# Optimization experiments

Measured on AMD Instinct MI355X. Metric: run time of the kernel, lower is better.

Reference implementation:

```python
import jax, jax.numpy as jnp
import numpy as np

NCHARS = 50000
NWORDS = 500000
NIC = 64      # ninput_char
NIW = 64      # ninput_word
NH = 128      # nhidden
NA = 5        # naction (nmapping_fn)
B = 65536     # batch size


def setup_inputs() -> dict:
    key = jax.random.key(0)
    ks = jax.random.split(key, 12)
    s = 0.05
    return {
        "x": jax.random.randint(ks[0], (B, 2), 0, NCHARS),
        "y": jax.random.randint(ks[1], (B,), 0, NWORDS),
        "cemb_table": jax.random.normal(ks[2], (NCHARS, NIC), jnp.float32) * s,
        "wemb_table": jax.random.normal(ks[3], (NWORDS, NIW), jnp.float32) * s,
        # Policy MLP: Linear(2*NIC -> NH), ReLU, Linear(NH -> NA), Softmax
        "Wp1": jax.random.normal(ks[4], (2 * NIC, NH), jnp.float32) * s,
        "bp1": jnp.zeros((NH,), jnp.float32),
        "Wp2": jax.random.normal(ks[5], (NH, NA), jnp.float32) * s,
        "bp2": jnp.zeros((NA,), jnp.float32),
        # NA expert MLPs, stacked: Linear(2*NIC -> NH), ReLU, Linear(NH -> NIW)
        "We1": jax.random.normal(ks[6], (NA, 2 * NIC, NH), jnp.float32) * s,
        "be1": jnp.zeros((NA, NH), jnp.float32),
        "We2": jax.random.normal(ks[7], (NA, NH, NIW), jnp.float32) * s,
        "be2": jnp.zeros((NA, NIW), jnp.float32),
    }


def reference(x, y, cemb_table, wemb_table, Wp1, bp1, Wp2, bp2, We1, be1, We2, be2):
    bsize = x.shape[0]
    # char_embs(x).view(bsize, -1): [B, 2*NIC]
    cembs = cemb_table[x].reshape(bsize, -1)

    # Policy (dropout off in eval): probs = softmax(relu(cembs@Wp1+bp1)@Wp2+bp2)
    # Categorical sampling over probs == categorical over the pre-softmax logits.
    logits = jnp.maximum(cembs @ Wp1 + bp1, 0.0) @ Wp2 + bp2
    action = jax.random.categorical(jax.random.key(42), logits)   # [B]
    action_mask = jax.nn.one_hot(action, NA, dtype=cembs.dtype)   # [B, NA]

    # Dense evaluation of all NA experts (matches the Python loop + stack)
    h = jnp.maximum(jnp.einsum('bd,adh->bah', cembs, We1) + be1, 0.0)  # [B, NA, NH]
    mapped = jnp.einsum('bah,aho->bao', h, We2) + be2                  # [B, NA, NIW]

    # sum(unsqueeze(mask,-1) * mapped, dim=1)
    out = jnp.einsum('ba,bao->bo', action_mask, mapped)               # [B, NIW]

    wemb = wemb_table[y]                                              # [B, NIW]
    return (out, wemb)
```

## Files before the change

### kernel.cpp

```cpp
#include <hip/hip_runtime.h>
#include <stdint.h>

#define B_N   65536
#define NIC   64
#define NIW   64
#define NH    128
#define NA    5
#define D2    128

#define PARTITIONABLE 1

#define P2_NCHUNK 51
#define P2_R      1286

typedef __attribute__((ext_vector_type(8))) short short8;
typedef __attribute__((ext_vector_type(4))) float f32x4;

__device__ __forceinline__ ushort f2bf(float f) {
  uint32_t u = __float_as_uint(f);
  uint32_t r = (u + 0x7FFFu + ((u >> 16) & 1u)) >> 16;
  return (ushort)r;
}

__device__ __forceinline__ void split2(float f, ushort& h, ushort& l) {
  h = f2bf(f);
  l = f2bf(f - __uint_as_float(((uint32_t)h) << 16));
}

__device__ __forceinline__ void threefry2x32_k042(uint32_t x0, uint32_t x1,
                                                  uint32_t& o0, uint32_t& o1) {
  const uint32_t ks0 = 0u;
  const uint32_t ks1 = 42u;
  const uint32_t ks2 = 0x1BD11BDAu ^ 0u ^ 42u;
  x0 += ks0; x1 += ks1;
#define TF_RND(r) { x0 += x1; x1 = (x1 << (r)) | (x1 >> (32 - (r))); x1 ^= x0; }
  TF_RND(13) TF_RND(15) TF_RND(26) TF_RND(6)
  x0 += ks1; x1 += ks2 + 1u;
  TF_RND(17) TF_RND(29) TF_RND(16) TF_RND(24)
  x0 += ks2; x1 += ks0 + 2u;
  TF_RND(13) TF_RND(15) TF_RND(26) TF_RND(6)
  x0 += ks0; x1 += ks1 + 3u;
  TF_RND(17) TF_RND(29) TF_RND(16) TF_RND(24)
  x0 += ks1; x1 += ks2 + 4u;
  TF_RND(13) TF_RND(15) TF_RND(26) TF_RND(6)
  x0 += ks2; x1 += ks0 + 5u;
#undef TF_RND
  o0 = x0; o1 = x1;
}

__device__ __forceinline__ float gumbel_at(uint32_t idx) {
  uint32_t bits;
#if PARTITIONABLE
  uint32_t a, b;
  threefry2x32_k042(0u, idx, a, b);
  bits = a ^ b;
#else
  const uint32_t HALF = (uint32_t)(B_N * NA) / 2u;
  uint32_t a, b;
  if (idx < HALF) { threefry2x32_k042(idx, idx + HALF, a, b); bits = a; }
  else            { threefry2x32_k042(idx - HALF, idx, a, b); bits = b; }
#endif
  const float f = __uint_as_float((bits >> 9) | 0x3f800000u) - 1.0f;
  const double u = (f == 0.0f) ? (double)0x1p-126 : (double)f;
  const float nl = (float)(-log(u));
  const float g  = (float)(-log((double)nl));
  return g;
}

__global__ __launch_bounds__(512, 4) void policy_kernel(
    const int* __restrict__ x, const int* __restrict__ y,
    const float* __restrict__ cemb, const float* __restrict__ wemb,
    const float* __restrict__ Wp1, const float* __restrict__ bp1,
    const float* __restrict__ Wp2, const float* __restrict__ bp2,
    float* __restrict__ out_wemb, int* __restrict__ action) {
  __shared__ __align__(16) ushort sW1h[16384];
  __shared__ __align__(16) ushort sW1l[16384];
  __shared__ __align__(16) float sW2t[NA][NH];
  __shared__ __align__(16) float sb1[NH];
  __shared__ __align__(16) float sbp2[8];

  const int tid = threadIdx.x;
  const int base = blockIdx.x * 128;

  {
    const int n = tid & 127, q = tid >> 7;
    const int fb = (n >> 4) * 4 + q;
    const int cc = n & 15;
#pragma unroll
    for (int grp = 0; grp < 4; grp++) {
      short8 ph, pl;
#pragma unroll
      for (int j = 0; j < 8; j++) {
        const int k = 32 * q + 8 * grp + j;
        ushort hh, ll;
        split2(Wp1[k * NH + n], hh, ll);
        ph[j] = (short)hh;
        pl[j] = (short)ll;
      }
      *(short8*)&sW1h[fb * 512 + (cc + 16 * grp) * 8] = ph;
      *(short8*)&sW1l[fb * 512 + (cc + 16 * grp) * 8] = pl;
    }
    if (tid < NH) sb1[tid] = bp1[tid];
    if (tid < NA * 32) {
      const int a = tid >> 5, k0 = (tid & 31) * 4;
#pragma unroll
      for (int j = 0; j < 4; j++) sW2t[a][k0 + j] = Wp2[(k0 + j) * NA + a];
    }
    if (tid < NA) sbp2[tid] = bp2[tid];
  }

  const int wave = tid >> 6, lane = tid & 63;
  const int c16 = lane & 15, h2 = lane >> 4;

  const int grow = base + wave * 16 + c16;
  const int xi0 = x[grow * 2], xi1 = x[grow * 2 + 1];
  short8 Ah[4], Al[4];
#pragma unroll
  for (int kt = 0; kt < 4; kt++) {
    const int xi = (kt < 2) ? xi0 : xi1;
    const float* src = cemb + (size_t)xi * NIC + (kt & 1) * 32 + h2 * 8;
    const float4 aa = *(const float4*)src;
    const float4 bb = *(const float4*)(src + 4);
    ushort hh, ll;
    short8 ph, pl;
    split2(aa.x, hh, ll); ph[0] = (short)hh; pl[0] = (short)ll;
    split2(aa.y, hh, ll); ph[1] = (short)hh; pl[1] = (short)ll;
    split2(aa.z, hh, ll); ph[2] = (short)hh; pl[2] = (short)ll;
    split2(aa.w, hh, ll); ph[3] = (short)hh; pl[3] = (short)ll;
    split2(bb.x, hh, ll); ph[4] = (short)hh; pl[4] = (short)ll;
    split2(bb.y, hh, ll); ph[5] = (short)hh; pl[5] = (short)ll;
    split2(bb.z, hh, ll); ph[6] = (short)hh; pl[6] = (short)ll;
    split2(bb.w, hh, ll); ph[7] = (short)hh; pl[7] = (short)ll;
    Ah[kt] = ph;
    Al[kt] = pl;
  }
  __syncthreads();

  float part[4][5];
#pragma unroll
  for (int r = 0; r < 4; r++)
#pragma unroll
    for (int a = 0; a < NA; a++) part[r][a] = 0.0f;

#pragma unroll
  for (int half = 0; half < 2; half++) {
    f32x4 acc[4];
#pragma unroll
    for (int c2 = 0; c2 < 4; c2++) {
      const float bv = sb1[(half * 4 + c2) * 16 + c16];
      acc[c2] = (f32x4){bv, bv, bv, bv};
    }
#pragma unroll
    for (int kt = 0; kt < 4; kt++) {
#pragma unroll
      for (int c2 = 0; c2 < 4; c2++) {
        const int fb = (half * 4 + c2) * 4 + kt;
        const short8 Bh = *(const short8*)&sW1h[fb * 512 + lane * 8];
        const short8 Bl = *(const short8*)&sW1l[fb * 512 + lane * 8];
        acc[c2] = __builtin_amdgcn_mfma_f32_16x16x32_bf16(Ah[kt], Bh, acc[c2], 0, 0, 0);
        acc[c2] = __builtin_amdgcn_mfma_f32_16x16x32_bf16(Al[kt], Bh, acc[c2], 0, 0, 0);
        acc[c2] = __builtin_amdgcn_mfma_f32_16x16x32_bf16(Ah[kt], Bl, acc[c2], 0, 0, 0);
      }
    }
#pragma unroll
    for (int c2 = 0; c2 < 4; c2++) {
      const int ct = half * 4 + c2;
      float w[NA];
#pragma unroll
      for (int a = 0; a < NA; a++) w[a] = sW2t[a][ct * 16 + c16];
#pragma unroll
      for (int r = 0; r < 4; r++) {
        const float hv = fmaxf(acc[c2][r], 0.0f);
#pragma unroll
        for (int a = 0; a < NA; a++) part[r][a] = fmaf(hv, w[a], part[r][a]);
      }
    }
  }

#pragma unroll
  for (int st = 1; st <= 8; st <<= 1) {
#pragma unroll
    for (int r = 0; r < 4; r++)
#pragma unroll
      for (int a = 0; a < NA; a++)
        part[r][a] += __shfl_xor(part[r][a], st);
  }

  float score0, score1;
  {
    const int r0_ = c16 / 5, a0_ = c16 - 5 * (c16 / 5);
    float lg = 0.0f;
#pragma unroll
    for (int r = 0; r < 4; r++)
#pragma unroll
      for (int a = 0; a < NA; a++)
        if (r0_ == r && a0_ == a) lg = part[r][a];
    const float logit = lg + sbp2[a0_];
    const int growr = base + wave * 16 + h2 * 4 + r0_;
    score0 = gumbel_at((uint32_t)(growr * NA + a0_)) + logit;
  }
  {
    const int a1_ = (c16 & 3) + 1;
    float lg = 0.0f;
#pragma unroll
    for (int a = 1; a < NA; a++)
      if (a1_ == a) lg = part[3][a];
    const float logit = lg + sbp2[a1_];
    const int growr = base + wave * 16 + h2 * 4 + 3;
    score1 = gumbel_at((uint32_t)(growr * NA + a1_)) + logit;
  }

  int best = 0;
  float bs = 0.0f;
#pragma unroll
  for (int a = 0; a < NA; a++) {
    const int idx = c16 * 5 + a;
    const int src = h2 * 16 + ((idx < 16) ? idx : (idx - 16));
    const float v0 = __shfl(score0, src);
    const float v1 = __shfl(score1, src);
    const float s = (idx < 16) ? v0 : v1;
    if (a == 0) bs = s;
    else if (s > bs) { bs = s; best = a; }
  }
  if (c16 < 4) action[base + wave * 16 + h2 * 4 + c16] = best;

#pragma unroll 1
  for (int i = tid; i < 128 * 16; i += 512) {
    const int row = i >> 4, seg = i & 15;
    ((float4*)out_wemb)[(size_t)(base + row) * 16 + seg] =
        ((const float4*)wemb)[(size_t)y[base + row] * 16 + seg];
  }
}

__global__ __launch_bounds__(512, 1) void expert_staged(
    const int* __restrict__ x, const float* __restrict__ cemb,
    const float* __restrict__ We1, const float* __restrict__ be1,
    const float* __restrict__ We2, const float* __restrict__ be2,
    const int* __restrict__ action, float* __restrict__ out) {
  __shared__ __align__(16) ushort sW1[32 * 512];
  __shared__ __align__(16) ushort sW2[16 * 512];
  __shared__ __align__(16) ushort sCt[8][4 * 512];
  __shared__ __align__(16) ushort sHt[8][4 * 512];
  __shared__ __align__(16) float sbe1[NH];
  __shared__ __align__(16) float sbe2[NIW];
  __shared__ int sList[P2_R];
  __shared__ int sCount;

  const int tid = threadIdx.x;
  const int a = blockIdx.x % NA;
  const int chunk = blockIdx.x / NA;
  const int rowBeg = chunk * P2_R;
  const int rowEnd = (rowBeg + P2_R < B_N) ? rowBeg + P2_R : B_N;

  if (tid == 0) sCount = 0;
  __syncthreads();

  for (int r = rowBeg + tid; r < rowEnd; r += 512)
    if (action[r] == a) sList[atomicAdd(&sCount, 1)] = r;

  {
    const float* W1g = We1 + (size_t)a * D2 * NH;
    const int n = tid & 127, q = tid >> 7;
    const int fb = (n >> 4) * 4 + q;
    const int cc = n & 15;
#pragma unroll
    for (int grp = 0; grp < 4; grp++) {
      short8 pk;
#pragma unroll
      for (int j = 0; j < 8; j++)
        pk[j] = (short)f2bf(W1g[(32 * q + 8 * grp + j) * NH + n]);
      *(short8*)&sW1[fb * 512 + (cc + 16 * grp) * 8] = pk;
    }
    if (tid < NH) sbe1[tid] = be1[a * NH + tid];
    if (tid < NIW) sbe2[tid] = be2[a * NIW + tid];
  }
  {
    const float* W2g = We2 + (size_t)a * NH * NIW;
    const int o = tid & 63, hq = tid >> 6;
    const int fb = (o >> 4) * 4 + (hq >> 1);
    const int cc = o & 15;
#pragma unroll
    for (int g2 = 0; g2 < 2; g2++) {
      const int grp = (hq & 1) * 2 + g2;
      short8 pk;
#pragma unroll
      for (int j = 0; j < 8; j++)
        pk[j] = (short)f2bf(W2g[(16 * hq + 8 * g2 + j) * NIW + o]);
      *(short8*)&sW2[fb * 512 + (cc + 16 * grp) * 8] = pk;
    }
  }
  __syncthreads();

  const int cnt = sCount;
  if (cnt == 0) return;

  const int wave = tid >> 6, lane = tid & 63;
  const int rowb = (lane >> 4) * 4;
  ushort* myCt = sCt[wave];
  ushort* myHt = sHt[wave];

#pragma unroll 1
  for (int t16 = wave * 16; t16 < cnt; t16 += 128) {
    {
      const int rt = lane >> 2, q = lane & 3;
      int li = t16 + rt;
      const int g = sList[(li < cnt) ? li : 0];
      const int xi = x[2 * g + (q >> 1)];
      const float4* src = (const float4*)(cemb + (size_t)xi * NIC + (q & 1) * 32);
#pragma unroll
      for (int grp = 0; grp < 4; grp++) {
        const float4 aa = src[2 * grp], bb = src[2 * grp + 1];
        short8 pk;
        pk[0] = (short)f2bf(aa.x); pk[1] = (short)f2bf(aa.y);
        pk[2] = (short)f2bf(aa.z); pk[3] = (short)f2bf(aa.w);
        pk[4] = (short)f2bf(bb.x); pk[5] = (short)f2bf(bb.y);
        pk[6] = (short)f2bf(bb.z); pk[7] = (short)f2bf(bb.w);
        *(short8*)&myCt[q * 512 + (rt + 16 * grp) * 8] = pk;
      }
    }

    short8 A[4];
#pragma unroll
    for (int kt = 0; kt < 4; kt++) A[kt] = *(const short8*)&myCt[kt * 512 + lane * 8];
#pragma unroll
    for (int ct = 0; ct < 8; ct++) {
      const int n = ct * 16 + (lane & 15);
      const float bv = sbe1[n];
      f32x4 acc = {bv, bv, bv, bv};
#pragma unroll
      for (int kt = 0; kt < 4; kt++) {
        const short8 Bf = *(const short8*)&sW1[(ct * 4 + kt) * 512 + lane * 8];
        acc = __builtin_amdgcn_mfma_f32_16x16x32_bf16(A[kt], Bf, acc, 0, 0, 0);
      }
      const int kt2 = n >> 5, grp2 = (n & 31) >> 3, j2 = n & 7;
#pragma unroll
      for (int r = 0; r < 4; r++)
        myHt[kt2 * 512 + ((rowb + r) + 16 * grp2) * 8 + j2] =
            f2bf(fmaxf(acc[r], 0.0f));
    }

    short8 A2[4];
#pragma unroll
    for (int kt = 0; kt < 4; kt++) A2[kt] = *(const short8*)&myHt[kt * 512 + lane * 8];
    int gr4[4];
#pragma unroll
    for (int r = 0; r < 4; r++) {
      const int li2 = t16 + rowb + r;
      gr4[r] = (li2 < cnt) ? sList[li2] : -1;
    }
#pragma unroll
    for (int ot = 0; ot < 4; ot++) {
      const int o = ot * 16 + (lane & 15);
      const float bv = sbe2[o];
      f32x4 o4 = {bv, bv, bv, bv};
#pragma unroll
      for (int kt = 0; kt < 4; kt++) {
        const short8 Bf = *(const short8*)&sW2[(ot * 4 + kt) * 512 + lane * 8];
        o4 = __builtin_amdgcn_mfma_f32_16x16x32_bf16(A2[kt], Bf, o4, 0, 0, 0);
      }
#pragma unroll
      for (int r = 0; r < 4; r++)
        if (gr4[r] >= 0) out[(size_t)gr4[r] * NIW + o] = o4[r];
    }
  }
}

extern "C" void kernel_launch(void* const* d_in, const int* in_sizes, int n_in,
                              void* d_out, int out_size, void* d_ws, size_t ws_size,
                              hipStream_t stream) {
  const int*   x    = (const int*)d_in[0];
  const int*   y    = (const int*)d_in[1];
  const float* cemb = (const float*)d_in[2];
  const float* wemb = (const float*)d_in[3];
  const float* Wp1  = (const float*)d_in[4];
  const float* bp1  = (const float*)d_in[5];
  const float* Wp2  = (const float*)d_in[6];
  const float* bp2  = (const float*)d_in[7];
  const float* We1  = (const float*)d_in[8];
  const float* be1  = (const float*)d_in[9];
  const float* We2  = (const float*)d_in[10];
  const float* be2  = (const float*)d_in[11];

  float* out      = (float*)d_out;
  float* out_wemb = out + (size_t)B_N * NIW;
  int*   action   = (int*)d_ws;

  policy_kernel<<<B_N / 128, 512, 0, stream>>>(
      x, y, cemb, wemb, Wp1, bp1, Wp2, bp2, out_wemb, action);
  expert_staged<<<NA * P2_NCHUNK, 512, 0, stream>>>(
      x, cemb, We1, be1, We2, be2, action, out);
}
```

Baseline: 42.35 us.

## Double block size to 1024 threads and load expert A-fragments directly from global

Both kernels move to 1024-thread blocks: the policy kernel handles 256 rows per block and the expert kernel runs 16 waves per chunk, with weight-staging loops re-split across the larger thread count. The expert kernel drops the per-wave shared-memory staging of char embeddings and builds the MFMA A fragments straight from global memory in registers. This is meant to cut LDS traffic and the amortised weight-conversion cost per block. In exchange it raises register pressure under tighter launch bounds and uses less coalesced per-lane global loads.

```diff
diff --git a/kernel.cpp b/kernel.cpp
--- a/kernel.cpp
+++ b/kernel.cpp
@@ -67,7 +67,7 @@
   return g;
 }
 
-__global__ __launch_bounds__(512, 4) void policy_kernel(
+__global__ __launch_bounds__(1024, 8) void policy_kernel(
     const int* __restrict__ x, const int* __restrict__ y,
     const float* __restrict__ cemb, const float* __restrict__ wemb,
     const float* __restrict__ Wp1, const float* __restrict__ bp1,
@@ -80,18 +80,20 @@
   __shared__ __align__(16) float sbp2[8];
 
   const int tid = threadIdx.x;
-  const int base = blockIdx.x * 128;
+  const int base = blockIdx.x * 256;
 
   {
     const int n = tid & 127, q = tid >> 7;
-    const int fb = (n >> 4) * 4 + q;
+    const int kt = q >> 1, gh = q & 1;
+    const int fb = (n >> 4) * 4 + kt;
     const int cc = n & 15;
 #pragma unroll
-    for (int grp = 0; grp < 4; grp++) {
+    for (int g = 0; g < 2; g++) {
+      const int grp = gh * 2 + g;
       short8 ph, pl;
 #pragma unroll
       for (int j = 0; j < 8; j++) {
-        const int k = 32 * q + 8 * grp + j;
+        const int k = 32 * kt + 8 * grp + j;
         ushort hh, ll;
         split2(Wp1[k * NH + n], hh, ll);
         ph[j] = (short)hh;
@@ -225,22 +227,21 @@
   if (c16 < 4) action[base + wave * 16 + h2 * 4 + c16] = best;
 
 #pragma unroll 1
-  for (int i = tid; i < 128 * 16; i += 512) {
+  for (int i = tid; i < 256 * 16; i += 1024) {
     const int row = i >> 4, seg = i & 15;
     ((float4*)out_wemb)[(size_t)(base + row) * 16 + seg] =
         ((const float4*)wemb)[(size_t)y[base + row] * 16 + seg];
   }
 }
 
-__global__ __launch_bounds__(512, 1) void expert_staged(
+__global__ __launch_bounds__(1024, 4) void expert_staged(
     const int* __restrict__ x, const float* __restrict__ cemb,
     const float* __restrict__ We1, const float* __restrict__ be1,
     const float* __restrict__ We2, const float* __restrict__ be2,
     const int* __restrict__ action, float* __restrict__ out) {
-  __shared__ __align__(16) ushort sW1[32 * 512];
-  __shared__ __align__(16) ushort sW2[16 * 512];
-  __shared__ __align__(16) ushort sCt[8][4 * 512];
-  __shared__ __align__(16) ushort sHt[8][4 * 512];
+  __shared__ __align__(16) ushort sW1[16384];
+  __shared__ __align__(16) ushort sW2[8192];
+  __shared__ __align__(16) ushort sHt[16][2048];
   __shared__ __align__(16) float sbe1[NH];
   __shared__ __align__(16) float sbe2[NIW];
   __shared__ int sList[P2_R];
@@ -255,20 +256,22 @@
   if (tid == 0) sCount = 0;
   __syncthreads();
 
-  for (int r = rowBeg + tid; r < rowEnd; r += 512)
+  for (int r = rowBeg + tid; r < rowEnd; r += 1024)
     if (action[r] == a) sList[atomicAdd(&sCount, 1)] = r;
 
   {
     const float* W1g = We1 + (size_t)a * D2 * NH;
     const int n = tid & 127, q = tid >> 7;
-    const int fb = (n >> 4) * 4 + q;
+    const int kt = q >> 1, gh = q & 1;
+    const int fb = (n >> 4) * 4 + kt;
     const int cc = n & 15;
 #pragma unroll
-    for (int grp = 0; grp < 4; grp++) {
+    for (int g = 0; g < 2; g++) {
+      const int grp = gh * 2 + g;
       short8 pk;
 #pragma unroll
       for (int j = 0; j < 8; j++)
-        pk[j] = (short)f2bf(W1g[(32 * q + 8 * grp + j) * NH + n]);
+        pk[j] = (short)f2bf(W1g[(32 * kt + 8 * grp + j) * NH + n]);
       *(short8*)&sW1[fb * 512 + (cc + 16 * grp) * 8] = pk;
     }
     if (tid < NH) sbe1[tid] = be1[a * NH + tid];
@@ -276,18 +279,15 @@
   }
   {
     const float* W2g = We2 + (size_t)a * NH * NIW;
-    const int o = tid & 63, hq = tid >> 6;
-    const int fb = (o >> 4) * 4 + (hq >> 1);
+    const int o = tid & 63, hq2 = tid >> 6;
+    const int kt = hq2 >> 2, grp = hq2 & 3;
+    const int fb = (o >> 4) * 4 + kt;
     const int cc = o & 15;
-#pragma unroll
-    for (int g2 = 0; g2 < 2; g2++) {
-      const int grp = (hq & 1) * 2 + g2;
-      short8 pk;
-#pragma unroll
-      for (int j = 0; j < 8; j++)
-        pk[j] = (short)f2bf(W2g[(16 * hq + 8 * g2 + j) * NIW + o]);
-      *(short8*)&sW2[fb * 512 + (cc + 16 * grp) * 8] = pk;
-    }
+    short8 pk;
+#pragma unroll
+    for (int j = 0; j < 8; j++)
+      pk[j] = (short)f2bf(W2g[(8 * hq2 + j) * NIW + o]);
+    *(short8*)&sW2[fb * 512 + (cc + 16 * grp) * 8] = pk;
   }
   __syncthreads();
 
@@ -295,42 +295,39 @@
   if (cnt == 0) return;
 
   const int wave = tid >> 6, lane = tid & 63;
-  const int rowb = (lane >> 4) * 4;
-  ushort* myCt = sCt[wave];
+  const int c16 = lane & 15, h2 = lane >> 4;
+  const int rowb = h2 * 4;
   ushort* myHt = sHt[wave];
 
 #pragma unroll 1
-  for (int t16 = wave * 16; t16 < cnt; t16 += 128) {
-    {
-      const int rt = lane >> 2, q = lane & 3;
-      int li = t16 + rt;
-      const int g = sList[(li < cnt) ? li : 0];
-      const int xi = x[2 * g + (q >> 1)];
-      const float4* src = (const float4*)(cemb + (size_t)xi * NIC + (q & 1) * 32);
-#pragma unroll
-      for (int grp = 0; grp < 4; grp++) {
-        const float4 aa = src[2 * grp], bb = src[2 * grp + 1];
-        short8 pk;
-        pk[0] = (short)f2bf(aa.x); pk[1] = (short)f2bf(aa.y);
-        pk[2] = (short)f2bf(aa.z); pk[3] = (short)f2bf(aa.w);
-        pk[4] = (short)f2bf(bb.x); pk[5] = (short)f2bf(bb.y);
-        pk[6] = (short)f2bf(bb.z); pk[7] = (short)f2bf(bb.w);
-        *(short8*)&myCt[q * 512 + (rt + 16 * grp) * 8] = pk;
-      }
-    }
-
-    short8 A[4];
-#pragma unroll
-    for (int kt = 0; kt < 4; kt++) A[kt] = *(const short8*)&myCt[kt * 512 + lane * 8];
+  for (int t16 = wave * 16; t16 < cnt; t16 += 256) {
+    const int slot = t16 + c16;
+    const int g = sList[(slot < cnt) ? slot : 0];
+    const int2 xi2 = ((const int2*)x)[g];
+    short8 Ae[4];
+#pragma unroll
+    for (int kt = 0; kt < 4; kt++) {
+      const float* src = cemb + (size_t)((kt < 2) ? xi2.x : xi2.y) * NIC +
+                         (kt & 1) * 32 + h2 * 8;
+      const float4 aa = *(const float4*)src;
+      const float4 bb = *(const float4*)(src + 4);
+      short8 pk;
+      pk[0] = (short)f2bf(aa.x); pk[1] = (short)f2bf(aa.y);
+      pk[2] = (short)f2bf(aa.z); pk[3] = (short)f2bf(aa.w);
+      pk[4] = (short)f2bf(bb.x); pk[5] = (short)f2bf(bb.y);
+      pk[6] = (short)f2bf(bb.z); pk[7] = (short)f2bf(bb.w);
+      Ae[kt] = pk;
+    }
+
 #pragma unroll
     for (int ct = 0; ct < 8; ct++) {
-      const int n = ct * 16 + (lane & 15);
+      const int n = ct * 16 + c16;
       const float bv = sbe1[n];
       f32x4 acc = {bv, bv, bv, bv};
 #pragma unroll
       for (int kt = 0; kt < 4; kt++) {
         const short8 Bf = *(const short8*)&sW1[(ct * 4 + kt) * 512 + lane * 8];
-        acc = __builtin_amdgcn_mfma_f32_16x16x32_bf16(A[kt], Bf, acc, 0, 0, 0);
+        acc = __builtin_amdgcn_mfma_f32_16x16x32_bf16(Ae[kt], Bf, acc, 0, 0, 0);
       }
       const int kt2 = n >> 5, grp2 = (n & 31) >> 3, j2 = n & 7;
 #pragma unroll
@@ -341,7 +338,8 @@
 
     short8 A2[4];
 #pragma unroll
-    for (int kt = 0; kt < 4; kt++) A2[kt] = *(const short8*)&myHt[kt * 512 + lane * 8];
+    for (int kt = 0; kt < 4; kt++)
+      A2[kt] = *(const short8*)&myHt[kt * 512 + lane * 8];
     int gr4[4];
 #pragma unroll
     for (int r = 0; r < 4; r++) {
@@ -350,7 +348,7 @@
     }
 #pragma unroll
     for (int ot = 0; ot < 4; ot++) {
-      const int o = ot * 16 + (lane & 15);
+      const int o = ot * 16 + c16;
       const float bv = sbe2[o];
       f32x4 o4 = {bv, bv, bv, bv};
 #pragma unroll
@@ -385,8 +383,8 @@
   float* out_wemb = out + (size_t)B_N * NIW;
   int*   action   = (int*)d_ws;
 
-  policy_kernel<<<B_N / 128, 512, 0, stream>>>(
+  policy_kernel<<<B_N / 256, 1024, 0, stream>>>(
       x, y, cemb, wemb, Wp1, bp1, Wp2, bp2, out_wemb, action);
-  expert_staged<<<NA * P2_NCHUNK, 512, 0, stream>>>(
+  expert_staged<<<NA * P2_NCHUNK, 1024, 0, stream>>>(
       x, cemb, We1, be1, We2, be2, action, out);
 }
```

After: 73.73 us. 1.74x slower.

## Shrink LDS footprint, load embeddings directly into MFMA fragments, interleave expert GEMMs

Applied to the files above, without the earlier changes.

The expert kernel no longer stages char embeddings through shared memory: each lane loads its MFMA A fragment straight from global memory and converts it to bf16 in registers. The hidden layer is computed in two halves, each feeding the second GEMM at once, which halves the per-wave hidden buffer. The row list becomes ushort, and the launch bound asks for 4 blocks per CU. The row chunk count is doubled so more, smaller blocks exist. The aim is higher occupancy and more blocks in flight. The stricter launch bound may cap VGPRs tightly enough to cause spills, and the weight restaging cost per block roughly doubles.

```diff
diff --git a/kernel.cpp b/kernel.cpp
--- a/kernel.cpp
+++ b/kernel.cpp
@@ -10,8 +10,8 @@
 
 #define PARTITIONABLE 1
 
-#define P2_NCHUNK 51
-#define P2_R      1286
+#define P2_NCHUNK 102
+#define P2_R      643
 
 typedef __attribute__((ext_vector_type(8))) short short8;
 typedef __attribute__((ext_vector_type(4))) float f32x4;
@@ -232,18 +232,17 @@
   }
 }
 
-__global__ __launch_bounds__(512, 1) void expert_staged(
+__global__ __launch_bounds__(512, 4) void expert_staged(
     const int* __restrict__ x, const float* __restrict__ cemb,
     const float* __restrict__ We1, const float* __restrict__ be1,
     const float* __restrict__ We2, const float* __restrict__ be2,
     const int* __restrict__ action, float* __restrict__ out) {
-  __shared__ __align__(16) ushort sW1[32 * 512];
-  __shared__ __align__(16) ushort sW2[16 * 512];
-  __shared__ __align__(16) ushort sCt[8][4 * 512];
-  __shared__ __align__(16) ushort sHt[8][4 * 512];
+  __shared__ __align__(16) ushort sW1[16384];
+  __shared__ __align__(16) ushort sW2[8192];
+  __shared__ __align__(16) ushort sHt[8][1024];
   __shared__ __align__(16) float sbe1[NH];
   __shared__ __align__(16) float sbe2[NIW];
-  __shared__ int sList[P2_R];
+  __shared__ ushort sList[P2_R];
   __shared__ int sCount;
 
   const int tid = threadIdx.x;
@@ -256,7 +255,7 @@
   __syncthreads();
 
   for (int r = rowBeg + tid; r < rowEnd; r += 512)
-    if (action[r] == a) sList[atomicAdd(&sCount, 1)] = r;
+    if (action[r] == a) sList[atomicAdd(&sCount, 1)] = (ushort)r;
 
   {
     const float* W1g = We1 + (size_t)a * D2 * NH;
@@ -295,72 +294,80 @@
   if (cnt == 0) return;
 
   const int wave = tid >> 6, lane = tid & 63;
-  const int rowb = (lane >> 4) * 4;
-  ushort* myCt = sCt[wave];
+  const int c16 = lane & 15, h2 = lane >> 4;
+  const int rowb = h2 * 4;
   ushort* myHt = sHt[wave];
 
 #pragma unroll 1
   for (int t16 = wave * 16; t16 < cnt; t16 += 128) {
-    {
-      const int rt = lane >> 2, q = lane & 3;
-      int li = t16 + rt;
-      const int g = sList[(li < cnt) ? li : 0];
-      const int xi = x[2 * g + (q >> 1)];
-      const float4* src = (const float4*)(cemb + (size_t)xi * NIC + (q & 1) * 32);
-#pragma unroll
-      for (int grp = 0; grp < 4; grp++) {
-        const float4 aa = src[2 * grp], bb = src[2 * grp + 1];
-        short8 pk;
-        pk[0] = (short)f2bf(aa.x); pk[1] = (short)f2bf(aa.y);
-        pk[2] = (short)f2bf(aa.z); pk[3] = (short)f2bf(aa.w);
-        pk[4] = (short)f2bf(bb.x); pk[5] = (short)f2bf(bb.y);
-        pk[6] = (short)f2bf(bb.z); pk[7] = (short)f2bf(bb.w);
-        *(short8*)&myCt[q * 512 + (rt + 16 * grp) * 8] = pk;
-      }
-    }
-
-    short8 A[4];
-#pragma unroll
-    for (int kt = 0; kt < 4; kt++) A[kt] = *(const short8*)&myCt[kt * 512 + lane * 8];
-#pragma unroll
-    for (int ct = 0; ct < 8; ct++) {
-      const int n = ct * 16 + (lane & 15);
-      const float bv = sbe1[n];
-      f32x4 acc = {bv, bv, bv, bv};
-#pragma unroll
-      for (int kt = 0; kt < 4; kt++) {
-        const short8 Bf = *(const short8*)&sW1[(ct * 4 + kt) * 512 + lane * 8];
-        acc = __builtin_amdgcn_mfma_f32_16x16x32_bf16(A[kt], Bf, acc, 0, 0, 0);
-      }
-      const int kt2 = n >> 5, grp2 = (n & 31) >> 3, j2 = n & 7;
-#pragma unroll
-      for (int r = 0; r < 4; r++)
-        myHt[kt2 * 512 + ((rowb + r) + 16 * grp2) * 8 + j2] =
-            f2bf(fmaxf(acc[r], 0.0f));
-    }
-
-    short8 A2[4];
-#pragma unroll
-    for (int kt = 0; kt < 4; kt++) A2[kt] = *(const short8*)&myHt[kt * 512 + lane * 8];
+    const int slot = t16 + c16;
+    const int g = sList[(slot < cnt) ? slot : 0];
+    const int2 xi2 = ((const int2*)x)[g];
+    short8 Ae[4];
+#pragma unroll
+    for (int kt = 0; kt < 4; kt++) {
+      const float* src = cemb + (size_t)((kt < 2) ? xi2.x : xi2.y) * NIC +
+                         (kt & 1) * 32 + h2 * 8;
+      const float4 aa = *(const float4*)src;
+      const float4 bb = *(const float4*)(src + 4);
+      short8 pk;
+      pk[0] = (short)f2bf(aa.x); pk[1] = (short)f2bf(aa.y);
+      pk[2] = (short)f2bf(aa.z); pk[3] = (short)f2bf(aa.w);
+      pk[4] = (short)f2bf(bb.x); pk[5] = (short)f2bf(bb.y);
+      pk[6] = (short)f2bf(bb.z); pk[7] = (short)f2bf(bb.w);
+      Ae[kt] = pk;
+    }
+
+    f32x4 o4[4];
+#pragma unroll
+    for (int ot = 0; ot < 4; ot++) {
+      const float bv = sbe2[ot * 16 + c16];
+      o4[ot] = (f32x4){bv, bv, bv, bv};
+    }
+
+#pragma unroll
+    for (int pass = 0; pass < 2; pass++) {
+#pragma unroll
+      for (int c2 = 0; c2 < 4; c2++) {
+        const int ct = pass * 4 + c2;
+        const int n = ct * 16 + c16;
+        const float bv = sbe1[n];
+        f32x4 ac = {bv, bv, bv, bv};
+#pragma unroll
+        for (int kt = 0; kt < 4; kt++) {
+          const short8 Bf = *(const short8*)&sW1[(ct * 4 + kt) * 512 + lane * 8];
+          ac = __builtin_amdgcn_mfma_f32_16x16x32_bf16(Ae[kt], Bf, ac, 0, 0, 0);
+        }
+        const int kt2 = n >> 5, grp2 = (n & 31) >> 3, j2 = n & 7;
+#pragma unroll
+        for (int r = 0; r < 4; r++)
+          myHt[(kt2 & 1) * 512 + ((rowb + r) + 16 * grp2) * 8 + j2] =
+              f2bf(fmaxf(ac[r], 0.0f));
+      }
+#pragma unroll
+      for (int i = 0; i < 2; i++) {
+        const int kt = pass * 2 + i;
+        const short8 A2 = *(const short8*)&myHt[i * 512 + lane * 8];
+#pragma unroll
+        for (int ot = 0; ot < 4; ot++) {
+          const short8 Bf = *(const short8*)&sW2[(ot * 4 + kt) * 512 + lane * 8];
+          o4[ot] = __builtin_amdgcn_mfma_f32_16x16x32_bf16(A2, Bf, o4[ot], 0, 0, 0);
+        }
+      }
+    }
+
     int gr4[4];
 #pragma unroll
     for (int r = 0; r < 4; r++) {
       const int li2 = t16 + rowb + r;
-      gr4[r] = (li2 < cnt) ? sList[li2] : -1;
+      gr4[r] = (li2 < cnt) ? (int)sList[li2] : -1;
     }
 #pragma unroll
     for (int ot = 0; ot < 4; ot++) {
-      const int o = ot * 16 + (lane & 15);
-      const float bv = sbe2[o];
-      f32x4 o4 = {bv, bv, bv, bv};
-#pragma unroll
-      for (int kt = 0; kt < 4; kt++) {
-        const short8 Bf = *(const short8*)&sW2[(ot * 4 + kt) * 512 + lane * 8];
-        o4 = __builtin_amdgcn_mfma_f32_16x16x32_bf16(A2[kt], Bf, o4, 0, 0, 0);
-      }
+      const int o = ot * 16 + c16;
 #pragma unroll
       for (int r = 0; r < 4; r++)
-        if (gr4[r] >= 0) out[(size_t)gr4[r] * NIW + o] = o4[r];
+        if (gr4[r] >= 0) out[(size_t)gr4[r] * NIW + o] = o4[ot][r];
     }
   }
 }
```

Result: slower. 69.59 us (+64.3%).
